# Performance work log

Hardware: AMD Instinct MI355X
Metric: run time of the kernel (lower is better)

The kernel has to match this reference:

```python
import jax, jax.numpy as jnp
import numpy as np

T, D, E, K = 16384, 4096, 64, 8
GUMBEL_TAU = 1.0
ROUTER_TEMP = 1.0
SELECT_TEMP = None  # falls back to router_temp, as in the module
EPS = 1e-06


def setup_inputs() -> dict:
    key = jax.random.key(0)
    k1, k2, k3 = jax.random.split(key, 3)
    h = jax.random.normal(k1, (T, D), dtype=jnp.float32)
    # eqx.nn.Linear weight: shape (out_features, in_features), uniform init scale
    W = jax.random.normal(k2, (E, D), dtype=jnp.float32) * (1.0 / np.sqrt(D))
    # uniform noise for Gumbel, matching minval=1e-6, maxval=1-1e-6
    u = jax.random.uniform(k3, (T, E), minval=EPS, maxval=1.0 - EPS, dtype=jnp.float32)
    return {"h": h, "W": W, "u": u}


def reference(h, W, u):
    # logits_clean = vmap(Linear)(h) = h @ W.T, shape (T, E)
    logits_clean = jnp.einsum("td,ed->te", h, W)

    t_mix = jnp.clip(jnp.float32(ROUTER_TEMP), EPS, None)
    probs = jax.nn.softmax(logits_clean / t_mix, axis=-1)

    sel_temp = ROUTER_TEMP if SELECT_TEMP is None else SELECT_TEMP
    t_sel = jnp.clip(jnp.float32(sel_temp), EPS, None)
    logits_sel = logits_clean / t_sel

    # training path: Gumbel noise g = -log(-log(u))
    g = -jnp.log(-jnp.log(u))
    logits_sel = logits_sel + GUMBEL_TAU * g

    # hard top-k mask per row (scatter of ones at top-k indices == one_hot().sum())
    _, idx = jax.lax.top_k(logits_sel, K)  # (T, K)
    rows = jnp.arange(logits_sel.shape[0])[:, None]
    mask_full = jnp.zeros(logits_sel.shape, dtype=bool).at[rows, idx].set(True)

    return (mask_full, probs, logits_clean, logits_sel)
```

## Files before the change

kernel.cpp:

```cpp
#include <hip/hip_runtime.h>
#include <hip/hip_bf16.h>
#include <math.h>
#include <stdint.h>

#define T_ROWS 16384
#define D_DIM  4096
#define E_EXP  64
#define TOPK   8

constexpr float W_SCALE   = 64.0f;
constexpr float INV_SCALE = 1.0f / 64.0f;

constexpr int BM   = 32;
constexpr int BK   = 32;
constexpr int KHALF = D_DIM / 2;
constexpr int NIT  = KHALF / BK;
constexpr int ABUF = 4096;
constexpr int BBUF = 8192;
constexpr int B_OFF = 3 * ABUF;
constexpr int LDS_TOT = B_OFF + 3 * BBUF;

typedef _Float16 f16x8 __attribute__((ext_vector_type(8)));
typedef __fp16   h16x2 __attribute__((ext_vector_type(2)));
typedef float    f32x4 __attribute__((ext_vector_type(4)));

__device__ __forceinline__ void gll16(const void* g, void* l) {
    __builtin_amdgcn_global_load_lds(
        (const __attribute__((address_space(1))) void*)g,
        (__attribute__((address_space(3))) void*)l, 16, 0, 0);
}
#define WAITV(n) asm volatile("s_waitcnt vmcnt(" #n ")" ::: "memory")
#define SB0()    __builtin_amdgcn_sched_barrier(0)

__global__ __launch_bounds__(256) void wprep_kernel(
    const float* __restrict__ W, _Float16* __restrict__ Wt)
{
    const int i  = blockIdx.x * 256 + threadIdx.x;
    const int e  = i >> 9;
    const int k8 = i & 511;
    const int k  = k8 << 3;
    const int t  = k >> 5;
    const int s  = (k >> 3) & 3;
    const float4 w0 = *(const float4*)&W[(size_t)e * D_DIM + k];
    const float4 w1 = *(const float4*)&W[(size_t)e * D_DIM + k + 4];
    const float xs[8] = {w0.x, w0.y, w0.z, w0.w, w1.x, w1.y, w1.z, w1.w};
    f16x8 hi, lo;
    #pragma unroll
    for (int j = 0; j < 8; ++j) {
        const float x = xs[j] * W_SCALE;
        const _Float16 hh = (_Float16)x;
        hi[j] = hh;
        lo[j] = (_Float16)(x - (float)hh);
    }
    const size_t o = (size_t)t * 4096 + e * 32 + ((s ^ (e & 3)) << 3);
    *(f16x8*)(Wt + o) = hi;
    *(f16x8*)(Wt + o + 2048) = lo;
}

__device__ __forceinline__ void cvt8(const float4 x0, const float4 x1,
                                     f16x8& hi, f16x8& lo) {
    const float xs[8] = {x0.x, x0.y, x0.z, x0.w, x1.x, x1.y, x1.z, x1.w};
    float hs[8], ls[8];
    #pragma unroll
    for (int j = 0; j < 8; ++j) {
        hs[j] = __uint_as_float(__float_as_uint(xs[j]) & 0xFFFFE000u);
        ls[j] = xs[j] - hs[j];
    }
    #pragma unroll
    for (int j = 0; j < 4; ++j) {
        const h16x2 ph = __builtin_amdgcn_cvt_pkrtz(hs[2 * j], hs[2 * j + 1]);
        const h16x2 pl = __builtin_amdgcn_cvt_pkrtz(ls[2 * j], ls[2 * j + 1]);
        hi[2 * j] = (_Float16)ph[0]; hi[2 * j + 1] = (_Float16)ph[1];
        lo[2 * j] = (_Float16)pl[0]; lo[2 * j + 1] = (_Float16)pl[1];
    }
}

__global__ __launch_bounds__(256, 4) void gemm_half_kernel(
    const float* __restrict__ h, const _Float16* __restrict__ Wt,
    float* __restrict__ out)
{
    __shared__ char smb[LDS_TOT];

    const int tid  = threadIdx.x;
    const int wv   = tid >> 6;
    const int lane = tid & 63;
    const int l15  = lane & 15;
    const int kg   = lane >> 4;
    const int wm   = wv >> 1;
    const int we   = wv & 1;
    const int row0 = blockIdx.x * BM;
    const int by   = blockIdx.y;
    const int kb   = by * KHALF;

    const int arow = wv * 8 + (lane >> 3);
    const char* gA = (const char*)h + ((size_t)(row0 + arow) * D_DIM + kb) * 4
                     + (((lane & 7) ^ (arow & 7)) << 4);
    const char* gB = (const char*)Wt + (size_t)by * 64 * 8192
                     + wv * 2048 + lane * 16;
    const int lB = B_OFF + wv * 2048;

    int aro[2];
    #pragma unroll
    for (int q = 0; q < 2; ++q)
        aro[q] = (wm * 16 + l15) * 128 + (((kg * 2 + q) ^ (l15 & 7)) << 4);
    int bro[2][2];
    #pragma unroll
    for (int sel = 0; sel < 2; ++sel)
        #pragma unroll
        for (int es = 0; es < 2; ++es) {
            const int e = we * 32 + es * 16 + l15;
            bro[sel][es] = B_OFF + sel * 4096 + e * 64 + ((kg ^ (e & 3)) << 4);
        }

    f32x4 acc[2] = {};
    float4 av[2];
    f16x8 bhf[2], blf[2];

    int aCur = 0, aNxt = ABUF, aStg = 2 * ABUF;
    int bCur = 0, bNxt = BBUF, bStg = 2 * BBUF;

    #define STAGE(t, aAdd, bAdd)                                      \
        { gll16(gA + (size_t)(t) * 128, smb + (aAdd) + wv * 1024);    \
          gll16(gB + (size_t)(t) * 8192,        smb + (bAdd) + lB);          \
          gll16(gB + (size_t)(t) * 8192 + 1024, smb + (bAdd) + lB + 1024); }

    #define DSREAD(aAdd, bAdd)                                                \
        { av[0] = *(const float4*)(smb + (aAdd) + aro[0]);                    \
          av[1] = *(const float4*)(smb + (aAdd) + aro[1]);                    \
          _Pragma("unroll")                                                   \
          for (int es = 0; es < 2; ++es) {                                    \
              bhf[es] = *(const f16x8*)(smb + (bAdd) + bro[0][es]);           \
              blf[es] = *(const f16x8*)(smb + (bAdd) + bro[1][es]);           \
          } }

    #define MFMAS()                                                           \
        { f16x8 ah, al;                                                       \
          cvt8(av[0], av[1], ah, al);                                         \
          _Pragma("unroll")                                                   \
          for (int es = 0; es < 2; ++es) {                                    \
              acc[es] = __builtin_amdgcn_mfma_f32_16x16x32_f16(ah, bhf[es], acc[es], 0, 0, 0); \
              acc[es] = __builtin_amdgcn_mfma_f32_16x16x32_f16(ah, blf[es], acc[es], 0, 0, 0); \
              acc[es] = __builtin_amdgcn_mfma_f32_16x16x32_f16(al, bhf[es], acc[es], 0, 0, 0); \
          } }

    #define ROT() { int t_;                                        \
        t_ = aCur; aCur = aNxt; aNxt = aStg; aStg = t_;            \
        t_ = bCur; bCur = bNxt; bNxt = bStg; bStg = t_; }

    STAGE(0, aCur, bCur)
    SB0();
    STAGE(1, aNxt, bNxt)
    SB0();
    WAITV(3);
    SB0();
    __builtin_amdgcn_s_barrier();

    for (int i = 0; i < NIT - 2; ++i) {
        DSREAD(aCur, bCur)
        STAGE(i + 2, aStg, bStg)
        SB0();
        __builtin_amdgcn_s_barrier();
        __builtin_amdgcn_s_setprio(1);
        MFMAS()
        __builtin_amdgcn_s_setprio(0);
        WAITV(3);
        SB0();
        __builtin_amdgcn_s_barrier();
        ROT();
    }
    DSREAD(aCur, bCur)
    __builtin_amdgcn_s_barrier();
    MFMAS()
    WAITV(0);
    SB0();
    __builtin_amdgcn_s_barrier();
    ROT();
    DSREAD(aCur, bCur)
    MFMAS()

    float* slot = out + (size_t)(2 + by) * T_ROWS * E_EXP;
    #pragma unroll
    for (int es = 0; es < 2; ++es)
        #pragma unroll
        for (int r = 0; r < 4; ++r)
            slot[(size_t)(row0 + wm * 16 + kg * 4 + r) * E_EXP
                 + we * 32 + es * 16 + l15] = acc[es][r];
}

__global__ __launch_bounds__(256) void epilogue_kernel(
    const float* __restrict__ u, float* __restrict__ out)
{
    const int row  = blockIdx.x * 4 + (threadIdx.x >> 6);
    const int lane = threadIdx.x & 63;
    const size_t te = (size_t)T_ROWS * E_EXP;
    const size_t idx = (size_t)row * E_EXP + lane;

    const float p0 = out[2 * te + idx];
    const float p1 = out[3 * te + idx];
    const float val = (p0 + p1) * INV_SCALE;

    out[2 * te + idx] = val;

    float m = val;
    #pragma unroll
    for (int off = 32; off; off >>= 1) m = fmaxf(m, __shfl_xor(m, off));
    const float p = expf(val - m);
    float ssum = p;
    #pragma unroll
    for (int off = 32; off; off >>= 1) ssum += __shfl_xor(ssum, off);
    out[1 * te + idx] = p / ssum;

    const float uv = u[idx];
    const float g = -logf(-logf(uv));
    const float sel = val + g;
    out[3 * te + idx] = sel;

    float v = sel;
    bool chosen = false;
    #pragma unroll
    for (int itk = 0; itk < TOPK; ++itk) {
        float mv = v;
        #pragma unroll
        for (int off = 32; off; off >>= 1) mv = fmaxf(mv, __shfl_xor(mv, off));
        const unsigned long long b = __ballot(v == mv);
        const int sl = __ffsll((long long)b) - 1;
        if (lane == sl) { chosen = true; v = -INFINITY; }
    }
    out[idx] = chosen ? 1.0f : 0.0f;
}

extern "C" void kernel_launch(void* const* d_in, const int* in_sizes, int n_in,
                              void* d_out, int out_size, void* d_ws, size_t ws_size,
                              hipStream_t stream) {
    const float* h = (const float*)d_in[0];
    const float* W = (const float*)d_in[1];
    const float* u = (const float*)d_in[2];
    float* out = (float*)d_out;

    _Float16* Wt = (_Float16*)d_ws;

    hipLaunchKernelGGL(wprep_kernel, dim3(E_EXP * D_DIM / 8 / 256), dim3(256),
                       0, stream, W, Wt);
    hipLaunchKernelGGL(gemm_half_kernel, dim3(T_ROWS / BM, 2), dim3(256),
                       0, stream, h, Wt, out);
    hipLaunchKernelGGL(epilogue_kernel, dim3(T_ROWS / 4), dim3(256),
                       0, stream, u, out);
}
```

Baseline: 86.33 us.

## Double GEMM row tile and split K into four partial slots

The GEMM block tile grows from 32 to 64 rows, so each W tile loaded into shared memory feeds twice as many rows. K is now split four ways instead of two, which keeps the grid at 1024 blocks. The four partial sums go into all four output slots and the epilogue adds them. B buffering drops from triple to double to fit the larger A buffers in LDS. The risks are higher register pressure from the doubled accumulators, and the epilogue now reads four partial planes instead of two.

```diff
diff --git a/kernel.cpp b/kernel.cpp
--- a/kernel.cpp
+++ b/kernel.cpp
@@ -11,14 +11,14 @@
 constexpr float W_SCALE   = 64.0f;
 constexpr float INV_SCALE = 1.0f / 64.0f;
 
-constexpr int BM   = 32;
+constexpr int BM   = 64;
 constexpr int BK   = 32;
-constexpr int KHALF = D_DIM / 2;
-constexpr int NIT  = KHALF / BK;
-constexpr int ABUF = 4096;
+constexpr int KQ   = D_DIM / 4;
+constexpr int NIT  = KQ / BK;
+constexpr int ABUF = 8192;
 constexpr int BBUF = 8192;
 constexpr int B_OFF = 3 * ABUF;
-constexpr int LDS_TOT = B_OFF + 3 * BBUF;
+constexpr int LDS_TOT = B_OFF + 2 * BBUF;
 
 typedef _Float16 f16x8 __attribute__((ext_vector_type(8)));
 typedef __fp16   h16x2 __attribute__((ext_vector_type(2)));
@@ -75,7 +75,7 @@
     }
 }
 
-__global__ __launch_bounds__(256, 4) void gemm_half_kernel(
+__global__ __launch_bounds__(256, 4) void gemm_q_kernel(
     const float* __restrict__ h, const _Float16* __restrict__ Wt,
     float* __restrict__ out)
 {
@@ -89,102 +89,124 @@
     const int wm   = wv >> 1;
     const int we   = wv & 1;
     const int row0 = blockIdx.x * BM;
-    const int by   = blockIdx.y;
-    const int kb   = by * KHALF;
-
-    const int arow = wv * 8 + (lane >> 3);
-    const char* gA = (const char*)h + ((size_t)(row0 + arow) * D_DIM + kb) * 4
-                     + (((lane & 7) ^ (arow & 7)) << 4);
-    const char* gB = (const char*)Wt + (size_t)by * 64 * 8192
+    const int q    = blockIdx.y;
+    const int kb   = q * KQ;
+
+    const char* gA[2]; int lA[2];
+    #pragma unroll
+    for (int p = 0; p < 2; ++p) {
+        const int row = wv * 16 + p * 8 + (lane >> 3);
+        gA[p] = (const char*)h + ((size_t)(row0 + row) * D_DIM + kb) * 4
+                + (((lane & 7) ^ (lane >> 3)) << 4);
+        lA[p] = wv * 2048 + p * 1024;
+    }
+    const char* gB = (const char*)Wt + (size_t)(q * 32) * 8192
                      + wv * 2048 + lane * 16;
-    const int lB = B_OFF + wv * 2048;
-
-    int aro[2];
-    #pragma unroll
-    for (int q = 0; q < 2; ++q)
-        aro[q] = (wm * 16 + l15) * 128 + (((kg * 2 + q) ^ (l15 & 7)) << 4);
+    const int lB = wv * 2048;
+
+    int aro[2][2];
+    #pragma unroll
+    for (int f = 0; f < 2; ++f)
+        #pragma unroll
+        for (int qq = 0; qq < 2; ++qq)
+            aro[f][qq] = (f * 32 + wm * 16 + l15) * 128
+                       + (((kg * 2 + qq) ^ (l15 & 7)) << 4);
     int bro[2][2];
     #pragma unroll
     for (int sel = 0; sel < 2; ++sel)
         #pragma unroll
         for (int es = 0; es < 2; ++es) {
             const int e = we * 32 + es * 16 + l15;
-            bro[sel][es] = B_OFF + sel * 4096 + e * 64 + ((kg ^ (e & 3)) << 4);
+            bro[sel][es] = sel * 4096 + e * 64 + ((kg ^ (e & 3)) << 4);
         }
 
-    f32x4 acc[2] = {};
-    float4 av[2];
+    f32x4 acc[2][2] = {};
+    float4 av[2][2];
     f16x8 bhf[2], blf[2];
 
     int aCur = 0, aNxt = ABUF, aStg = 2 * ABUF;
-    int bCur = 0, bNxt = BBUF, bStg = 2 * BBUF;
-
-    #define STAGE(t, aAdd, bAdd)                                      \
-        { gll16(gA + (size_t)(t) * 128, smb + (aAdd) + wv * 1024);    \
-          gll16(gB + (size_t)(t) * 8192,        smb + (bAdd) + lB);          \
-          gll16(gB + (size_t)(t) * 8192 + 1024, smb + (bAdd) + lB + 1024); }
-
-    #define DSREAD(aAdd, bAdd)                                                \
-        { av[0] = *(const float4*)(smb + (aAdd) + aro[0]);                    \
-          av[1] = *(const float4*)(smb + (aAdd) + aro[1]);                    \
+
+    #define STAGE_A(t, aAdd)                                          \
+        { _Pragma("unroll")                                           \
+          for (int p = 0; p < 2; ++p)                                 \
+              gll16(gA[p] + (size_t)(t) * 128, smb + (aAdd) + lA[p]); }
+    #define STAGE_B(t, par)                                           \
+        { gll16(gB + (size_t)(t) * 8192,        smb + B_OFF + (par) * BBUF + lB); \
+          gll16(gB + (size_t)(t) * 8192 + 1024, smb + B_OFF + (par) * BBUF + lB + 1024); }
+
+    #define DSREAD(aAdd, par)                                                 \
+        { _Pragma("unroll")                                                   \
+          for (int f = 0; f < 2; ++f) {                                       \
+              av[f][0] = *(const float4*)(smb + (aAdd) + aro[f][0]);          \
+              av[f][1] = *(const float4*)(smb + (aAdd) + aro[f][1]);          \
+          }                                                                   \
           _Pragma("unroll")                                                   \
           for (int es = 0; es < 2; ++es) {                                    \
-              bhf[es] = *(const f16x8*)(smb + (bAdd) + bro[0][es]);           \
-              blf[es] = *(const f16x8*)(smb + (bAdd) + bro[1][es]);           \
+              bhf[es] = *(const f16x8*)(smb + B_OFF + (par) * BBUF + bro[0][es]); \
+              blf[es] = *(const f16x8*)(smb + B_OFF + (par) * BBUF + bro[1][es]); \
           } }
 
     #define MFMAS()                                                           \
-        { f16x8 ah, al;                                                       \
-          cvt8(av[0], av[1], ah, al);                                         \
+        { f16x8 ah[2], al[2];                                                 \
+          cvt8(av[0][0], av[0][1], ah[0], al[0]);                             \
+          cvt8(av[1][0], av[1][1], ah[1], al[1]);                             \
           _Pragma("unroll")                                                   \
-          for (int es = 0; es < 2; ++es) {                                    \
-              acc[es] = __builtin_amdgcn_mfma_f32_16x16x32_f16(ah, bhf[es], acc[es], 0, 0, 0); \
-              acc[es] = __builtin_amdgcn_mfma_f32_16x16x32_f16(ah, blf[es], acc[es], 0, 0, 0); \
-              acc[es] = __builtin_amdgcn_mfma_f32_16x16x32_f16(al, bhf[es], acc[es], 0, 0, 0); \
-          } }
-
-    #define ROT() { int t_;                                        \
-        t_ = aCur; aCur = aNxt; aNxt = aStg; aStg = t_;            \
-        t_ = bCur; bCur = bNxt; bNxt = bStg; bStg = t_; }
-
-    STAGE(0, aCur, bCur)
-    SB0();
-    STAGE(1, aNxt, bNxt)
-    SB0();
-    WAITV(3);
+          for (int f = 0; f < 2; ++f)                                         \
+              _Pragma("unroll")                                               \
+              for (int es = 0; es < 2; ++es) {                                \
+                  acc[f][es] = __builtin_amdgcn_mfma_f32_16x16x32_f16(ah[f], bhf[es], acc[f][es], 0, 0, 0); \
+                  acc[f][es] = __builtin_amdgcn_mfma_f32_16x16x32_f16(ah[f], blf[es], acc[f][es], 0, 0, 0); \
+                  acc[f][es] = __builtin_amdgcn_mfma_f32_16x16x32_f16(al[f], bhf[es], acc[f][es], 0, 0, 0); \
+              } }
+
+    #define ROT() { int t_ = aCur; aCur = aNxt; aNxt = aStg; aStg = t_; }
+
+    STAGE_A(0, aCur)
+    SB0();
+    STAGE_B(0, 0)
+    SB0();
+    STAGE_A(1, aNxt)
+    SB0();
+    WAITV(2);
     SB0();
     __builtin_amdgcn_s_barrier();
 
     for (int i = 0; i < NIT - 2; ++i) {
-        DSREAD(aCur, bCur)
-        STAGE(i + 2, aStg, bStg)
+        DSREAD(aCur, i & 1)
+        STAGE_B(i + 1, (i + 1) & 1)
+        SB0();
+        STAGE_A(i + 2, aStg)
         SB0();
         __builtin_amdgcn_s_barrier();
         __builtin_amdgcn_s_setprio(1);
         MFMAS()
         __builtin_amdgcn_s_setprio(0);
-        WAITV(3);
+        WAITV(2);
         SB0();
         __builtin_amdgcn_s_barrier();
         ROT();
     }
-    DSREAD(aCur, bCur)
+    DSREAD(aCur, (NIT - 2) & 1)
+    STAGE_B(NIT - 1, (NIT - 1) & 1)
+    SB0();
     __builtin_amdgcn_s_barrier();
     MFMAS()
     WAITV(0);
     SB0();
     __builtin_amdgcn_s_barrier();
     ROT();
-    DSREAD(aCur, bCur)
+    DSREAD(aCur, (NIT - 1) & 1)
     MFMAS()
 
-    float* slot = out + (size_t)(2 + by) * T_ROWS * E_EXP;
-    #pragma unroll
-    for (int es = 0; es < 2; ++es)
-        #pragma unroll
-        for (int r = 0; r < 4; ++r)
-            slot[(size_t)(row0 + wm * 16 + kg * 4 + r) * E_EXP
-                 + we * 32 + es * 16 + l15] = acc[es][r];
+    float* slot = out + (size_t)q * T_ROWS * E_EXP;
+    #pragma unroll
+    for (int f = 0; f < 2; ++f)
+        #pragma unroll
+        for (int es = 0; es < 2; ++es)
+            #pragma unroll
+            for (int r = 0; r < 4; ++r)
+                slot[(size_t)(row0 + f * 32 + wm * 16 + kg * 4 + r) * E_EXP
+                     + we * 32 + es * 16 + l15] = acc[f][es][r];
 }
 
 __global__ __launch_bounds__(256) void epilogue_kernel(
@@ -195,9 +217,11 @@
     const size_t te = (size_t)T_ROWS * E_EXP;
     const size_t idx = (size_t)row * E_EXP + lane;
 
-    const float p0 = out[2 * te + idx];
-    const float p1 = out[3 * te + idx];
-    const float val = (p0 + p1) * INV_SCALE;
+    const float p0 = out[0 * te + idx];
+    const float p1 = out[1 * te + idx];
+    const float p2 = out[2 * te + idx];
+    const float p3 = out[3 * te + idx];
+    const float val = (((p0 + p1) + p2) + p3) * INV_SCALE;
 
     out[2 * te + idx] = val;
 
@@ -241,7 +265,7 @@
 
     hipLaunchKernelGGL(wprep_kernel, dim3(E_EXP * D_DIM / 8 / 256), dim3(256),
                        0, stream, W, Wt);
-    hipLaunchKernelGGL(gemm_half_kernel, dim3(T_ROWS / BM, 2), dim3(256),
+    hipLaunchKernelGGL(gemm_q_kernel, dim3(T_ROWS / BM, 4), dim3(256),
                        0, stream, h, Wt, out);
     hipLaunchKernelGGL(epilogue_kernel, dim3(T_ROWS / 4), dim3(256),
                        0, stream, u, out);
```

Measured after the change: 79.02 us. 1.09x faster.
